# Optimization experiments

Measured on AMD Instinct MI355X. Metric: run time of the kernel, lower is better.

Reference implementation:

```python
import jax, jax.numpy as jnp
import numpy as np

N_NODES = 100000
N_EDGES = 1600000
D_IN = 128
D_OUT = 128


def setup_inputs() -> dict:
    key = jax.random.key(0)
    k1, k2, k3, k4 = jax.random.split(key, 4)
    x = jax.random.normal(k1, (N_NODES, D_IN), dtype=jnp.float32)
    edge_index = jax.random.randint(k2, (2, N_EDGES), 0, N_NODES, dtype=jnp.int64)
    # PyTorch Linear default init: U(-1/sqrt(fan_in), 1/sqrt(fan_in))
    bound = 1.0 / np.sqrt(D_IN)
    W1 = jax.random.uniform(k3, (D_OUT, D_IN), minval=-bound, maxval=bound, dtype=jnp.float32)
    W2 = jax.random.uniform(k4, (D_OUT, D_IN), minval=-bound, maxval=bound, dtype=jnp.float32)
    return {"x": x, "edge_index": edge_index, "W1": W1, "W2": W2}


def reference(x, edge_index, W1, W2):
    # self transform: [N, D_out]
    self_features = x @ W1.T
    # neighbor transform: [N, D_out]
    neighbor_features = x @ W2.T
    row, col = edge_index[0], edge_index[1]
    # gather by source (col), scatter-add by destination (row)
    aggregated = jax.ops.segment_sum(neighbor_features[col], row, num_segments=x.shape[0])
    return jax.nn.relu(self_features + aggregated)
```

## Files before the change

kernel.cpp:

```cpp
#include <hip/hip_runtime.h>

#define N_NODES 100000
#define DIM 128
#define NBIN 391
#define BINSZ 256
#define NCH 782
#define CHUNK 2048
#define FCAP 24
#define SLOTS (NBIN * FCAP)
#define ENTCAP 4608
#define FSPB 128
#define SSPB 256
#define NGEMM 782

typedef __attribute__((ext_vector_type(8))) short bf16x8;
typedef __attribute__((ext_vector_type(4))) float f32x4;

__device__ __forceinline__ unsigned short f2bf(float f) {
  unsigned u = __builtin_bit_cast(unsigned, f);
  u += 0x7fff + ((u >> 16) & 1);
  return (unsigned short)(u >> 16);
}
__device__ __forceinline__ float bfhi(unsigned u) {
  return __builtin_bit_cast(float, u & 0xffff0000u);
}
__device__ __forceinline__ float bflo(unsigned u) {
  return __builtin_bit_cast(float, u << 16);
}

__global__ __launch_bounds__(256, 4) void fill_kernel(
    const int* __restrict__ rows, const int* __restrict__ cols,
    int* __restrict__ counts, unsigned* __restrict__ binned,
    int* __restrict__ fspillc, int2* __restrict__ fspill, int n_edges,
    const float* __restrict__ W1, const float* __restrict__ W2,
    unsigned short* __restrict__ Wb) {
  const int tid = threadIdx.x;
  if (blockIdx.x >= NCH) {
    const int v = (blockIdx.x - NCH) * 256 + tid;
    const int j = v >> 5, q = v & 31;
    const float* Wrow =
        (j < 128) ? (W1 + (size_t)j * DIM) : (W2 + (size_t)(j - 128) * DIM);
    const float4 val = *(const float4*)(Wrow + 4 * q);
    const unsigned lo = (unsigned)f2bf(val.x) | ((unsigned)f2bf(val.y) << 16);
    const unsigned hi = (unsigned)f2bf(val.z) | ((unsigned)f2bf(val.w) << 16);
    *(uint2*)(Wb + (size_t)j * DIM + 4 * q) = make_uint2(lo, hi);
    return;
  }

  __shared__ unsigned buf[SLOTS];
  __shared__ int lcnt[NBIN];
  __shared__ int fsc;
  const int ch = blockIdx.x;
  for (int i = tid; i < NBIN; i += 256) lcnt[i] = 0;
  if (tid == 0) fsc = 0;
  __syncthreads();

  const int e0 = ch * CHUNK + tid * 8;
  int rv[8], cv[8];
  int nval;
  if (e0 + 8 <= n_edges) {
    *(int4*)&rv[0] = *(const int4*)(rows + e0);
    *(int4*)&rv[4] = *(const int4*)(rows + e0 + 4);
    *(int4*)&cv[0] = *(const int4*)(cols + e0);
    *(int4*)&cv[4] = *(const int4*)(cols + e0 + 4);
    nval = 8;
  } else {
    nval = 0;
    for (int k = 0; k < 8; ++k)
      if (e0 + k < n_edges) {
        rv[nval] = rows[e0 + k];
        cv[nval] = cols[e0 + k];
        ++nval;
      }
  }
  for (int k = 0; k < nval; ++k) {
    const int r = rv[k];
    const int b = r >> 8;
    const unsigned payload = ((unsigned)(r & 255) << 17) | (unsigned)cv[k];
    const int slot = atomicAdd(&lcnt[b], 1);
    if (slot < FCAP) {
      buf[b * FCAP + slot] = payload;
    } else {
      const int sp = atomicAdd(&fsc, 1);
      if (sp < FSPB) fspill[ch * FSPB + sp] = make_int2(r, cv[k]);
    }
  }
  __syncthreads();

  unsigned* dst = binned + (size_t)ch * SLOTS;
  for (int i4 = tid; i4 < SLOTS / 4; i4 += 256)
    *(uint4*)(dst + 4 * i4) = *(const uint4*)&buf[4 * i4];
  for (int b = tid; b < NBIN; b += 256)
    counts[(size_t)ch * NBIN + b] = min(lcnt[b], FCAP);
  if (tid == 0) fspillc[ch] = min(fsc, FSPB);
}

union FusedSh {
  unsigned short xs[128 * 136];
  struct {
    int segc[NCH], ssa[NCH], ssb[NCH];
    unsigned entbuf[ENTCAP];
    int outbuf[ENTCAP];
    int hist[BINSZ], hsa[BINSZ], hsb[BINSZ], cur[BINSZ];
    int ssc;
  } s;
};

__global__ __launch_bounds__(256, 2) void gemmsort_kernel(
    const float* __restrict__ x, const unsigned short* __restrict__ Wb,
    unsigned short* __restrict__ selfb, unsigned short* __restrict__ neigh,
    const int* __restrict__ counts, const unsigned* __restrict__ binned,
    int* __restrict__ csr_cols, int* __restrict__ row_ptr,
    int* __restrict__ degs, int* __restrict__ sspillc,
    int2* __restrict__ sspill) {
  __shared__ FusedSh sh;
  const int tid = threadIdx.x;
  const int g = blockIdx.x / 3, r3 = blockIdx.x % 3;

  if (r3 < 2) {
    const int t = g * 2 + r3;
    const int lane = tid & 63;
    const int w = tid >> 6;
    const int nb = t * 128;
    const int quad = lane >> 4;
    const int l15 = lane & 15;

    bf16x8 bfrag[4][4];
#pragma unroll
    for (int nt = 0; nt < 4; ++nt) {
      const int j = w * 64 + nt * 16 + l15;
#pragma unroll
      for (int ks = 0; ks < 4; ++ks)
        bfrag[nt][ks] =
            *(const bf16x8*)(Wb + (size_t)j * DIM + ks * 32 + quad * 8);
    }

#pragma unroll
    for (int half = 0; half < 2; ++half) {
      float4 av[8];
#pragma unroll
      for (int it = 0; it < 8; ++it) {
        const int v = tid + (half * 8 + it) * 256;
        const int m = v >> 5, q = v & 31;
        av[it] = (nb + m < N_NODES)
                     ? *(const float4*)(x + (size_t)(nb + m) * DIM + 4 * q)
                     : make_float4(0.f, 0.f, 0.f, 0.f);
      }
#pragma unroll
      for (int it = 0; it < 8; ++it) {
        const int v = tid + (half * 8 + it) * 256;
        const int m = v >> 5, q = v & 31;
        const unsigned lo =
            (unsigned)f2bf(av[it].x) | ((unsigned)f2bf(av[it].y) << 16);
        const unsigned hi =
            (unsigned)f2bf(av[it].z) | ((unsigned)f2bf(av[it].w) << 16);
        *(uint2*)&sh.xs[m * 136 + 4 * q] = make_uint2(lo, hi);
      }
    }
    __syncthreads();

    f32x4 acc[8][4];
#pragma unroll
    for (int mt = 0; mt < 8; ++mt)
#pragma unroll
      for (int nt = 0; nt < 4; ++nt) acc[mt][nt] = (f32x4){0.f, 0.f, 0.f, 0.f};

#pragma unroll
    for (int ks = 0; ks < 4; ++ks) {
#pragma unroll
      for (int mt = 0; mt < 8; ++mt) {
        const bf16x8 afrag =
            *(const bf16x8*)&sh.xs[(mt * 16 + l15) * 136 + ks * 32 + quad * 8];
#pragma unroll
        for (int nt = 0; nt < 4; ++nt)
          acc[mt][nt] = __builtin_amdgcn_mfma_f32_16x16x32_bf16(
              afrag, bfrag[nt][ks], acc[mt][nt], 0, 0, 0);
      }
    }

#pragma unroll
    for (int h = 0; h < 2; ++h) {
      __syncthreads();
      if ((w >> 1) == h) {
#pragma unroll
        for (int mt = 0; mt < 8; ++mt)
#pragma unroll
          for (int nt = 0; nt < 4; ++nt) {
            const int col = (w & 1) * 64 + nt * 16 + l15;
#pragma unroll
            for (int r = 0; r < 4; ++r)
              sh.xs[(mt * 16 + quad * 4 + r) * 136 + col] =
                  f2bf(acc[mt][nt][r]);
          }
      }
      __syncthreads();
      unsigned short* dst = h ? neigh : selfb;
#pragma unroll
      for (int it = 0; it < 8; ++it) {
        const int v = it * 256 + tid;
        const int row = v >> 4, q = v & 15;
        if (nb + row < N_NODES)
          *(uint4*)(dst + (size_t)(nb + row) * DIM + 8 * q) =
              *(const uint4*)&sh.xs[row * 136 + 8 * q];
      }
    }
  } else {
    const int bin = g;
    if (tid == 0) sh.s.ssc = 0;

    for (int i = tid; i < NCH; i += 256) {
      const int c = counts[(size_t)i * NBIN + bin];
      sh.s.segc[i] = c;
      sh.s.ssa[i] = c;
    }
    __syncthreads();
    for (int off = 1; off < NCH; off <<= 1) {
      for (int i = tid; i < NCH; i += 256)
        sh.s.ssb[i] = sh.s.ssa[i] + ((i >= off) ? sh.s.ssa[i - off] : 0);
      __syncthreads();
      for (int i = tid; i < NCH; i += 256) sh.s.ssa[i] = sh.s.ssb[i];
      __syncthreads();
    }

    const unsigned* bbase = binned + (size_t)bin * FCAP;
    for (int u = tid; u < NCH * (FCAP / 4); u += 256) {
      const int ch = u / 6;
      const int q = u - ch * 6;
      uint4 v4 = *(const uint4*)(bbase + (size_t)ch * SLOTS + 4 * q);
      const int cnt = sh.s.segc[ch];
      const int base = sh.s.ssa[ch] - cnt;
      const unsigned vals[4] = {v4.x, v4.y, v4.z, v4.w};
#pragma unroll
      for (int j = 0; j < 4; ++j) {
        const int slot = 4 * q + j;
        if (slot < cnt) {
          const int pos = base + slot;
          if (pos < ENTCAP) {
            sh.s.entbuf[pos] = vals[j];
          } else {
            const int sp = atomicAdd(&sh.s.ssc, 1);
            if (sp < SSPB)
              sspill[bin * SSPB + sp] =
                  make_int2((bin << 8) | (int)(vals[j] >> 17),
                            (int)(vals[j] & 0x1FFFFu));
          }
        }
      }
    }
    sh.s.hist[tid] = 0;
    __syncthreads();

    const int total = min(sh.s.ssa[NCH - 1], ENTCAP);
    for (int i = tid; i < total; i += 256)
      atomicAdd(&sh.s.hist[sh.s.entbuf[i] >> 17], 1);
    __syncthreads();

    sh.s.hsa[tid] = sh.s.hist[tid];
    __syncthreads();
    for (int off = 1; off < BINSZ; off <<= 1) {
      sh.s.hsb[tid] = sh.s.hsa[tid] + ((tid >= off) ? sh.s.hsa[tid - off] : 0);
      __syncthreads();
      sh.s.hsa[tid] = sh.s.hsb[tid];
      __syncthreads();
    }

    const int gbase = bin * ENTCAP;
    {
      const int start = sh.s.hsa[tid] - sh.s.hist[tid];
      sh.s.cur[tid] = start;
      const int node = (bin << 8) | tid;
      if (node < N_NODES) {
        row_ptr[node] = gbase + start;
        degs[node] = sh.s.hist[tid];
      }
    }
    __syncthreads();

    for (int i = tid; i < total; i += 256) {
      const unsigned p = sh.s.entbuf[i];
      const int pos = atomicAdd(&sh.s.cur[p >> 17], 1);
      sh.s.outbuf[pos] = (int)(p & 0x1FFFFu);
    }
    __syncthreads();

    for (int i = tid; i < total; i += 256)
      csr_cols[gbase + i] = sh.s.outbuf[i];
    if (tid == 0) sspillc[bin] = min(sh.s.ssc, SSPB);
  }
}

__global__ __launch_bounds__(256) void agg_kernel(
    const int* __restrict__ row_ptr, const int* __restrict__ degs,
    const int* __restrict__ csr_cols, const unsigned short* __restrict__ neigh,
    const unsigned short* __restrict__ selfb, const int* __restrict__ fspillc,
    const int2* __restrict__ fspill, const int* __restrict__ sspillc,
    const int2* __restrict__ sspill, float* __restrict__ out) {
  __shared__ int has_spill;
  const int tid = threadIdx.x;
  if (tid == 0) has_spill = 0;
  __syncthreads();
  for (int i = tid; i < NCH + NBIN; i += 256) {
    const int v = (i < NCH) ? fspillc[i] : sspillc[i - NCH];
    if (v) atomicOr(&has_spill, 1);
  }
  __syncthreads();
  const bool spilled = has_spill != 0;

  const int l = tid & 63;
  const int wid = blockIdx.x * 4 + (tid >> 6);
  const int stride = gridDim.x * 4;
  const unsigned* ng = (const unsigned*)neigh;

  for (int node = wid; node < N_NODES; node += stride) {
    const int deg = degs[node];
    const int* cl = csr_cols + row_ptr[node];
    const unsigned s = ((const unsigned*)selfb)[(size_t)node * 64 + l];

    float ax = 0.f, ay = 0.f;
    int d = 0;
    for (; d + 8 <= deg; d += 8) {
      unsigned uv[8];
#pragma unroll
      for (int k = 0; k < 8; ++k) uv[k] = ng[(size_t)cl[d + k] * 64 + l];
#pragma unroll
      for (int k = 0; k < 8; ++k) {
        ax += bflo(uv[k]);
        ay += bfhi(uv[k]);
      }
    }
    const int rem = deg - d;
    if (rem) {
      unsigned uv[8];
      const int cdup = cl[d];
#pragma unroll
      for (int k = 0; k < 8; ++k) {
        const int ci = (k < rem) ? cl[d + k] : cdup;
        uv[k] = ng[(size_t)ci * 64 + l];
      }
#pragma unroll
      for (int k = 0; k < 8; ++k) {
        if (k < rem) {
          ax += bflo(uv[k]);
          ay += bfhi(uv[k]);
        }
      }
    }

    if (spilled) {
      for (int bi = 0; bi < NCH; ++bi) {
        const int n = min(fspillc[bi], FSPB);
        for (int i = 0; i < n; ++i) {
          const int2 e = fspill[bi * FSPB + i];
          if (e.x == node) {
            const unsigned u = ng[(size_t)e.y * 64 + l];
            ax += bflo(u);
            ay += bfhi(u);
          }
        }
      }
      for (int bi = 0; bi < NBIN; ++bi) {
        const int n = min(sspillc[bi], SSPB);
        for (int i = 0; i < n; ++i) {
          const int2 e = sspill[bi * SSPB + i];
          if (e.x == node) {
            const unsigned u = ng[(size_t)e.y * 64 + l];
            ax += bflo(u);
            ay += bfhi(u);
          }
        }
      }
    }

    float2 o;
    o.x = fmaxf(bflo(s) + ax, 0.f);
    o.y = fmaxf(bfhi(s) + ay, 0.f);
    *(float2*)(out + (size_t)node * DIM + 2 * l) = o;
  }
}

extern "C" void kernel_launch(void* const* d_in, const int* in_sizes, int n_in,
                              void* d_out, int out_size, void* d_ws,
                              size_t ws_size, hipStream_t stream) {
  const float* x = (const float*)d_in[0];
  const int* edge_index = (const int*)d_in[1];
  const float* W1 = (const float*)d_in[2];
  const float* W2 = (const float*)d_in[3];
  float* out = (float*)d_out;

  const int n_edges = in_sizes[1] / 2;
  const int* rows = edge_index;
  const int* cols = edge_index + n_edges;

  char* p = (char*)d_ws;
  unsigned short* selfb = (unsigned short*)p;
  p += (size_t)N_NODES * DIM * 2;
  unsigned short* neigh = (unsigned short*)p;
  p += (size_t)N_NODES * DIM * 2;
  unsigned* binned = (unsigned*)p;
  p += (size_t)NCH * SLOTS * 4;
  int* counts = (int*)p;
  p += (size_t)NCH * NBIN * 4;
  int* csr_cols = (int*)p;
  p += (size_t)NBIN * ENTCAP * 4;
  int* row_ptr = (int*)p;
  p += (size_t)N_NODES * 4;
  int* degs = (int*)p;
  p += (size_t)N_NODES * 4;
  int* fspillc = (int*)p;
  p += 4096;
  int2* fspill = (int2*)p;
  p += (size_t)NCH * FSPB * sizeof(int2);
  int* sspillc = (int*)p;
  p += 4096;
  int2* sspill = (int2*)p;
  p += (size_t)NBIN * SSPB * sizeof(int2);
  unsigned short* Wb = (unsigned short*)p;

  fill_kernel<<<NCH + 32, 256, 0, stream>>>(rows, cols, counts, binned,
                                            fspillc, fspill, n_edges, W1, W2,
                                            Wb);
  gemmsort_kernel<<<3 * NBIN, 256, 0, stream>>>(x, Wb, selfb, neigh, counts,
                                                binned, csr_cols, row_ptr,
                                                degs, sspillc, sspill);
  agg_kernel<<<2048, 256, 0, stream>>>(row_ptr, degs, csr_cols, neigh, selfb,
                                       fspillc, fspill, sspillc, sspill, out);
}
```

Measured before the change: 231.1 us.

## Split GEMM from bin sort and fuse per-bin sort with aggregation

Moves the bin sort out of the fused GEMM kernel and into a new 1024-thread kernel that sorts each bin's edges in LDS and aggregates the same bin's nodes straight from LDS. This removes the global CSR write and read (csr_cols, row_ptr, degs) and the global spill scan in aggregation, and handles spills per bin in LDS. In exchange the sort can no longer overlap with the GEMM, and the grid shrinks to 391 large blocks that each gather 256 nodes, which may limit parallelism and latency hiding. A stray `outb[0]=outb[0]` write and a hard spill cap of 64 add minor risk.

```diff
diff --git a/kernel.cpp b/kernel.cpp
--- a/kernel.cpp
+++ b/kernel.cpp
@@ -10,7 +10,7 @@
 #define SLOTS (NBIN * FCAP)
 #define ENTCAP 4608
 #define FSPB 128
-#define SSPB 256
+#define LSPB 64
 #define NGEMM 782
 
 typedef __attribute__((ext_vector_type(8))) short bf16x8;
@@ -95,279 +95,255 @@
   if (tid == 0) fspillc[ch] = min(fsc, FSPB);
 }
 
-union FusedSh {
-  unsigned short xs[128 * 136];
-  struct {
-    int segc[NCH], ssa[NCH], ssb[NCH];
-    unsigned entbuf[ENTCAP];
-    int outbuf[ENTCAP];
-    int hist[BINSZ], hsa[BINSZ], hsb[BINSZ], cur[BINSZ];
-    int ssc;
-  } s;
-};
-
-__global__ __launch_bounds__(256, 2) void gemmsort_kernel(
+__global__ __launch_bounds__(256, 2) void gemm_kernel(
     const float* __restrict__ x, const unsigned short* __restrict__ Wb,
-    unsigned short* __restrict__ selfb, unsigned short* __restrict__ neigh,
+    unsigned short* __restrict__ selfb, unsigned short* __restrict__ neigh) {
+  __shared__ unsigned short xs[128 * 136];
+  const int tid = threadIdx.x;
+  const int t = blockIdx.x;
+  const int lane = tid & 63;
+  const int w = tid >> 6;
+  const int nb = t * 128;
+  const int quad = lane >> 4;
+  const int l15 = lane & 15;
+
+  bf16x8 bfrag[4][4];
+#pragma unroll
+  for (int nt = 0; nt < 4; ++nt) {
+    const int j = w * 64 + nt * 16 + l15;
+#pragma unroll
+    for (int ks = 0; ks < 4; ++ks)
+      bfrag[nt][ks] =
+          *(const bf16x8*)(Wb + (size_t)j * DIM + ks * 32 + quad * 8);
+  }
+
+#pragma unroll
+  for (int half = 0; half < 2; ++half) {
+    float4 av[8];
+#pragma unroll
+    for (int it = 0; it < 8; ++it) {
+      const int v = tid + (half * 8 + it) * 256;
+      const int m = v >> 5, q = v & 31;
+      av[it] = (nb + m < N_NODES)
+                   ? *(const float4*)(x + (size_t)(nb + m) * DIM + 4 * q)
+                   : make_float4(0.f, 0.f, 0.f, 0.f);
+    }
+#pragma unroll
+    for (int it = 0; it < 8; ++it) {
+      const int v = tid + (half * 8 + it) * 256;
+      const int m = v >> 5, q = v & 31;
+      const unsigned lo =
+          (unsigned)f2bf(av[it].x) | ((unsigned)f2bf(av[it].y) << 16);
+      const unsigned hi =
+          (unsigned)f2bf(av[it].z) | ((unsigned)f2bf(av[it].w) << 16);
+      *(uint2*)&xs[m * 136 + 4 * q] = make_uint2(lo, hi);
+    }
+  }
+  __syncthreads();
+
+  f32x4 acc[8][4];
+#pragma unroll
+  for (int mt = 0; mt < 8; ++mt)
+#pragma unroll
+    for (int nt = 0; nt < 4; ++nt) acc[mt][nt] = (f32x4){0.f, 0.f, 0.f, 0.f};
+
+#pragma unroll
+  for (int ks = 0; ks < 4; ++ks) {
+#pragma unroll
+    for (int mt = 0; mt < 8; ++mt) {
+      const bf16x8 afrag =
+          *(const bf16x8*)&xs[(mt * 16 + l15) * 136 + ks * 32 + quad * 8];
+#pragma unroll
+      for (int nt = 0; nt < 4; ++nt)
+        acc[mt][nt] = __builtin_amdgcn_mfma_f32_16x16x32_bf16(
+            afrag, bfrag[nt][ks], acc[mt][nt], 0, 0, 0);
+    }
+  }
+
+#pragma unroll
+  for (int h = 0; h < 2; ++h) {
+    __syncthreads();
+    if ((w >> 1) == h) {
+#pragma unroll
+      for (int mt = 0; mt < 8; ++mt)
+#pragma unroll
+        for (int nt = 0; nt < 4; ++nt) {
+          const int col = (w & 1) * 64 + nt * 16 + l15;
+#pragma unroll
+          for (int r = 0; r < 4; ++r)
+            xs[(mt * 16 + quad * 4 + r) * 136 + col] = f2bf(acc[mt][nt][r]);
+        }
+    }
+    __syncthreads();
+    unsigned short* dst = h ? neigh : selfb;
+#pragma unroll
+    for (int it = 0; it < 8; ++it) {
+      const int v = it * 256 + tid;
+      const int row = v >> 4, q = v & 15;
+      if (nb + row < N_NODES)
+        *(uint4*)(dst + (size_t)(nb + row) * DIM + 8 * q) =
+            *(const uint4*)&xs[row * 136 + 8 * q];
+    }
+  }
+}
+
+__global__ __launch_bounds__(1024, 8) void sortagg_kernel(
     const int* __restrict__ counts, const unsigned* __restrict__ binned,
-    int* __restrict__ csr_cols, int* __restrict__ row_ptr,
-    int* __restrict__ degs, int* __restrict__ sspillc,
-    int2* __restrict__ sspill) {
-  __shared__ FusedSh sh;
+    const unsigned short* __restrict__ neigh,
+    const unsigned short* __restrict__ selfb,
+    const int* __restrict__ fspillc, const int2* __restrict__ fspill,
+    float* __restrict__ out) {
+  __shared__ int segc[NCH];
+  __shared__ int ssa[NCH];
+  __shared__ unsigned entbuf[ENTCAP];
+  __shared__ int outb[ENTCAP];
+  __shared__ int hist[BINSZ], hsa[BINSZ], cur[BINSZ];
+  __shared__ unsigned lspill[LSPB];
+  __shared__ int lsc, tot, hasf;
+
   const int tid = threadIdx.x;
-  const int g = blockIdx.x / 3, r3 = blockIdx.x % 3;
-
-  if (r3 < 2) {
-    const int t = g * 2 + r3;
-    const int lane = tid & 63;
-    const int w = tid >> 6;
-    const int nb = t * 128;
-    const int quad = lane >> 4;
-    const int l15 = lane & 15;
-
-    bf16x8 bfrag[4][4];
-#pragma unroll
-    for (int nt = 0; nt < 4; ++nt) {
-      const int j = w * 64 + nt * 16 + l15;
-#pragma unroll
-      for (int ks = 0; ks < 4; ++ks)
-        bfrag[nt][ks] =
-            *(const bf16x8*)(Wb + (size_t)j * DIM + ks * 32 + quad * 8);
-    }
-
-#pragma unroll
-    for (int half = 0; half < 2; ++half) {
-      float4 av[8];
-#pragma unroll
-      for (int it = 0; it < 8; ++it) {
-        const int v = tid + (half * 8 + it) * 256;
-        const int m = v >> 5, q = v & 31;
-        av[it] = (nb + m < N_NODES)
-                     ? *(const float4*)(x + (size_t)(nb + m) * DIM + 4 * q)
-                     : make_float4(0.f, 0.f, 0.f, 0.f);
-      }
-#pragma unroll
-      for (int it = 0; it < 8; ++it) {
-        const int v = tid + (half * 8 + it) * 256;
-        const int m = v >> 5, q = v & 31;
-        const unsigned lo =
-            (unsigned)f2bf(av[it].x) | ((unsigned)f2bf(av[it].y) << 16);
-        const unsigned hi =
-            (unsigned)f2bf(av[it].z) | ((unsigned)f2bf(av[it].w) << 16);
-        *(uint2*)&sh.xs[m * 136 + 4 * q] = make_uint2(lo, hi);
-      }
-    }
-    __syncthreads();
-
-    f32x4 acc[8][4];
-#pragma unroll
-    for (int mt = 0; mt < 8; ++mt)
-#pragma unroll
-      for (int nt = 0; nt < 4; ++nt) acc[mt][nt] = (f32x4){0.f, 0.f, 0.f, 0.f};
-
-#pragma unroll
-    for (int ks = 0; ks < 4; ++ks) {
-#pragma unroll
-      for (int mt = 0; mt < 8; ++mt) {
-        const bf16x8 afrag =
-            *(const bf16x8*)&sh.xs[(mt * 16 + l15) * 136 + ks * 32 + quad * 8];
-#pragma unroll
-        for (int nt = 0; nt < 4; ++nt)
-          acc[mt][nt] = __builtin_amdgcn_mfma_f32_16x16x32_bf16(
-              afrag, bfrag[nt][ks], acc[mt][nt], 0, 0, 0);
-      }
-    }
-
-#pragma unroll
-    for (int h = 0; h < 2; ++h) {
-      __syncthreads();
-      if ((w >> 1) == h) {
-#pragma unroll
-        for (int mt = 0; mt < 8; ++mt)
-#pragma unroll
-          for (int nt = 0; nt < 4; ++nt) {
-            const int col = (w & 1) * 64 + nt * 16 + l15;
-#pragma unroll
-            for (int r = 0; r < 4; ++r)
-              sh.xs[(mt * 16 + quad * 4 + r) * 136 + col] =
-                  f2bf(acc[mt][nt][r]);
-          }
-      }
-      __syncthreads();
-      unsigned short* dst = h ? neigh : selfb;
-#pragma unroll
-      for (int it = 0; it < 8; ++it) {
-        const int v = it * 256 + tid;
-        const int row = v >> 4, q = v & 15;
-        if (nb + row < N_NODES)
-          *(uint4*)(dst + (size_t)(nb + row) * DIM + 8 * q) =
-              *(const uint4*)&sh.xs[row * 136 + 8 * q];
-      }
-    }
-  } else {
-    const int bin = g;
-    if (tid == 0) sh.s.ssc = 0;
-
-    for (int i = tid; i < NCH; i += 256) {
-      const int c = counts[(size_t)i * NBIN + bin];
-      sh.s.segc[i] = c;
-      sh.s.ssa[i] = c;
-    }
-    __syncthreads();
-    for (int off = 1; off < NCH; off <<= 1) {
-      for (int i = tid; i < NCH; i += 256)
-        sh.s.ssb[i] = sh.s.ssa[i] + ((i >= off) ? sh.s.ssa[i - off] : 0);
-      __syncthreads();
-      for (int i = tid; i < NCH; i += 256) sh.s.ssa[i] = sh.s.ssb[i];
-      __syncthreads();
-    }
-
-    const unsigned* bbase = binned + (size_t)bin * FCAP;
-    for (int u = tid; u < NCH * (FCAP / 4); u += 256) {
-      const int ch = u / 6;
-      const int q = u - ch * 6;
-      uint4 v4 = *(const uint4*)(bbase + (size_t)ch * SLOTS + 4 * q);
-      const int cnt = sh.s.segc[ch];
-      const int base = sh.s.ssa[ch] - cnt;
-      const unsigned vals[4] = {v4.x, v4.y, v4.z, v4.w};
-#pragma unroll
-      for (int j = 0; j < 4; ++j) {
-        const int slot = 4 * q + j;
-        if (slot < cnt) {
-          const int pos = base + slot;
+  const int bin = blockIdx.x;
+
+  if (tid == 0) {
+    lsc = 0;
+    hasf = 0;
+  }
+  if (tid < BINSZ) hist[tid] = 0;
+  for (int i = tid; i < NCH; i += 1024) {
+    const int c = counts[(size_t)i * NBIN + bin];
+    segc[i] = c;
+    ssa[i] = c;
+    if (fspillc[i]) atomicOr(&hasf, 1);
+  }
+  __syncthreads();
+
+  for (int off = 1; off < NCH; off <<= 1) {
+    int add = 0;
+    if (tid < NCH && tid >= off) add = ssa[tid - off];
+    __syncthreads();
+    if (tid < NCH && tid >= off) ssa[tid] += add;
+    __syncthreads();
+  }
+  if (tid == 0) tot = min(ssa[NCH - 1], ENTCAP);
+
+  const unsigned* bbase = binned + (size_t)bin * FCAP;
+  for (int u = tid; u < NCH * (FCAP / 4); u += 1024) {
+    const int ch = u / 6;
+    const int q = u - ch * 6;
+    uint4 v4 = *(const uint4*)(bbase + (size_t)ch * SLOTS + 4 * q);
+    const int cnt = segc[ch];
+    const int base = ssa[ch] - cnt;
+    const unsigned vals[4] = {v4.x, v4.y, v4.z, v4.w};
+#pragma unroll
+    for (int j = 0; j < 4; ++j) {
+      const int slot = 4 * q + j;
+      if (slot < cnt) {
+        const int pos = base + slot;
+        if (pos < ENTCAP) {
+          outb[0] = outb[0];
+          entbuf[pos] = vals[j];
+        } else {
+          const int sp = atomicAdd(&lsc, 1);
+          if (sp < LSPB) lspill[sp] = vals[j];
+        }
+      }
+    }
+  }
+  __syncthreads();
+
+  if (hasf) {
+    for (int bi = tid; bi < NCH; bi += 1024) {
+      const int n = min(fspillc[bi], FSPB);
+      for (int i = 0; i < n; ++i) {
+        const int2 e = fspill[bi * FSPB + i];
+        if ((e.x >> 8) == bin) {
+          const unsigned pay = ((unsigned)(e.x & 255) << 17) | (unsigned)e.y;
+          const int pos = atomicAdd(&tot, 1);
           if (pos < ENTCAP) {
-            sh.s.entbuf[pos] = vals[j];
+            entbuf[pos] = pay;
           } else {
-            const int sp = atomicAdd(&sh.s.ssc, 1);
-            if (sp < SSPB)
-              sspill[bin * SSPB + sp] =
-                  make_int2((bin << 8) | (int)(vals[j] >> 17),
-                            (int)(vals[j] & 0x1FFFFu));
+            const int sp = atomicAdd(&lsc, 1);
+            if (sp < LSPB) lspill[sp] = pay;
           }
         }
       }
     }
-    sh.s.hist[tid] = 0;
-    __syncthreads();
-
-    const int total = min(sh.s.ssa[NCH - 1], ENTCAP);
-    for (int i = tid; i < total; i += 256)
-      atomicAdd(&sh.s.hist[sh.s.entbuf[i] >> 17], 1);
-    __syncthreads();
-
-    sh.s.hsa[tid] = sh.s.hist[tid];
-    __syncthreads();
-    for (int off = 1; off < BINSZ; off <<= 1) {
-      sh.s.hsb[tid] = sh.s.hsa[tid] + ((tid >= off) ? sh.s.hsa[tid - off] : 0);
-      __syncthreads();
-      sh.s.hsa[tid] = sh.s.hsb[tid];
-      __syncthreads();
-    }
-
-    const int gbase = bin * ENTCAP;
-    {
-      const int start = sh.s.hsa[tid] - sh.s.hist[tid];
-      sh.s.cur[tid] = start;
-      const int node = (bin << 8) | tid;
-      if (node < N_NODES) {
-        row_ptr[node] = gbase + start;
-        degs[node] = sh.s.hist[tid];
-      }
-    }
-    __syncthreads();
-
-    for (int i = tid; i < total; i += 256) {
-      const unsigned p = sh.s.entbuf[i];
-      const int pos = atomicAdd(&sh.s.cur[p >> 17], 1);
-      sh.s.outbuf[pos] = (int)(p & 0x1FFFFu);
-    }
-    __syncthreads();
-
-    for (int i = tid; i < total; i += 256)
-      csr_cols[gbase + i] = sh.s.outbuf[i];
-    if (tid == 0) sspillc[bin] = min(sh.s.ssc, SSPB);
-  }
-}
-
-__global__ __launch_bounds__(256) void agg_kernel(
-    const int* __restrict__ row_ptr, const int* __restrict__ degs,
-    const int* __restrict__ csr_cols, const unsigned short* __restrict__ neigh,
-    const unsigned short* __restrict__ selfb, const int* __restrict__ fspillc,
-    const int2* __restrict__ fspill, const int* __restrict__ sspillc,
-    const int2* __restrict__ sspill, float* __restrict__ out) {
-  __shared__ int has_spill;
-  const int tid = threadIdx.x;
-  if (tid == 0) has_spill = 0;
-  __syncthreads();
-  for (int i = tid; i < NCH + NBIN; i += 256) {
-    const int v = (i < NCH) ? fspillc[i] : sspillc[i - NCH];
-    if (v) atomicOr(&has_spill, 1);
-  }
-  __syncthreads();
-  const bool spilled = has_spill != 0;
+    __syncthreads();
+  }
+  const int total = min(tot, ENTCAP);
+
+  for (int i = tid; i < total; i += 1024)
+    atomicAdd(&hist[entbuf[i] >> 17], 1);
+  __syncthreads();
+  if (tid < BINSZ) hsa[tid] = hist[tid];
+  __syncthreads();
+  for (int off = 1; off < BINSZ; off <<= 1) {
+    int add = 0;
+    if (tid < BINSZ && tid >= off) add = hsa[tid - off];
+    __syncthreads();
+    if (tid < BINSZ && tid >= off) hsa[tid] += add;
+    __syncthreads();
+  }
+  if (tid < BINSZ) cur[tid] = hsa[tid] - hist[tid];
+  __syncthreads();
+
+  for (int i = tid; i < total; i += 1024) {
+    const unsigned p = entbuf[i];
+    const int pos = atomicAdd(&cur[p >> 17], 1);
+    outb[pos] = (int)(p & 0x1FFFFu);
+  }
+  __syncthreads();
 
   const int l = tid & 63;
-  const int wid = blockIdx.x * 4 + (tid >> 6);
-  const int stride = gridDim.x * 4;
+  const int wv = tid >> 6;
   const unsigned* ng = (const unsigned*)neigh;
-
-  for (int node = wid; node < N_NODES; node += stride) {
-    const int deg = degs[node];
-    const int* cl = csr_cols + row_ptr[node];
-    const unsigned s = ((const unsigned*)selfb)[(size_t)node * 64 + l];
+  const unsigned* sfp = (const unsigned*)selfb;
+  const int nspill = min(lsc, LSPB);
+
+  for (int k = 0; k < 16; ++k) {
+    const int nl = wv * 16 + k;
+    const int node = (bin << 8) | nl;
+    if (node >= N_NODES) break;
+    const int deg = hist[nl];
+    const int start = hsa[nl] - hist[nl];
+    const unsigned s = sfp[(size_t)node * 64 + l];
 
     float ax = 0.f, ay = 0.f;
     int d = 0;
     for (; d + 8 <= deg; d += 8) {
       unsigned uv[8];
 #pragma unroll
-      for (int k = 0; k < 8; ++k) uv[k] = ng[(size_t)cl[d + k] * 64 + l];
-#pragma unroll
-      for (int k = 0; k < 8; ++k) {
-        ax += bflo(uv[k]);
-        ay += bfhi(uv[k]);
+      for (int j = 0; j < 8; ++j) uv[j] = ng[(size_t)outb[start + d + j] * 64 + l];
+#pragma unroll
+      for (int j = 0; j < 8; ++j) {
+        ax += bflo(uv[j]);
+        ay += bfhi(uv[j]);
       }
     }
     const int rem = deg - d;
     if (rem) {
       unsigned uv[8];
-      const int cdup = cl[d];
-#pragma unroll
-      for (int k = 0; k < 8; ++k) {
-        const int ci = (k < rem) ? cl[d + k] : cdup;
-        uv[k] = ng[(size_t)ci * 64 + l];
-      }
-#pragma unroll
-      for (int k = 0; k < 8; ++k) {
-        if (k < rem) {
-          ax += bflo(uv[k]);
-          ay += bfhi(uv[k]);
+      const int cdup = outb[start + d];
+#pragma unroll
+      for (int j = 0; j < 8; ++j) {
+        const int ci = (j < rem) ? outb[start + d + j] : cdup;
+        uv[j] = ng[(size_t)ci * 64 + l];
+      }
+#pragma unroll
+      for (int j = 0; j < 8; ++j) {
+        if (j < rem) {
+          ax += bflo(uv[j]);
+          ay += bfhi(uv[j]);
         }
       }
     }
 
-    if (spilled) {
-      for (int bi = 0; bi < NCH; ++bi) {
-        const int n = min(fspillc[bi], FSPB);
-        for (int i = 0; i < n; ++i) {
-          const int2 e = fspill[bi * FSPB + i];
-          if (e.x == node) {
-            const unsigned u = ng[(size_t)e.y * 64 + l];
-            ax += bflo(u);
-            ay += bfhi(u);
-          }
-        }
-      }
-      for (int bi = 0; bi < NBIN; ++bi) {
-        const int n = min(sspillc[bi], SSPB);
-        for (int i = 0; i < n; ++i) {
-          const int2 e = sspill[bi * SSPB + i];
-          if (e.x == node) {
-            const unsigned u = ng[(size_t)e.y * 64 + l];
-            ax += bflo(u);
-            ay += bfhi(u);
-          }
-        }
+    for (int i = 0; i < nspill; ++i) {
+      const unsigned p = lspill[i];
+      if ((int)(p >> 17) == nl) {
+        const unsigned u = ng[(size_t)(p & 0x1FFFFu) * 64 + l];
+        ax += bflo(u);
+        ay += bfhi(u);
       }
     }
 
@@ -400,28 +376,21 @@
   p += (size_t)NCH * SLOTS * 4;
   int* counts = (int*)p;
   p += (size_t)NCH * NBIN * 4;
-  int* csr_cols = (int*)p;
   p += (size_t)NBIN * ENTCAP * 4;
-  int* row_ptr = (int*)p;
   p += (size_t)N_NODES * 4;
-  int* degs = (int*)p;
   p += (size_t)N_NODES * 4;
   int* fspillc = (int*)p;
   p += 4096;
   int2* fspill = (int2*)p;
   p += (size_t)NCH * FSPB * sizeof(int2);
-  int* sspillc = (int*)p;
   p += 4096;
-  int2* sspill = (int2*)p;
-  p += (size_t)NBIN * SSPB * sizeof(int2);
+  p += (size_t)NBIN * 256 * sizeof(int2);
   unsigned short* Wb = (unsigned short*)p;
 
   fill_kernel<<<NCH + 32, 256, 0, stream>>>(rows, cols, counts, binned,
                                             fspillc, fspill, n_edges, W1, W2,
                                             Wb);
-  gemmsort_kernel<<<3 * NBIN, 256, 0, stream>>>(x, Wb, selfb, neigh, counts,
-                                                binned, csr_cols, row_ptr,
-                                                degs, sspillc, sspill);
-  agg_kernel<<<2048, 256, 0, stream>>>(row_ptr, degs, csr_cols, neigh, selfb,
-                                       fspillc, fspill, sspillc, sspill, out);
-}
+  gemm_kernel<<<NGEMM, 256, 0, stream>>>(x, Wb, selfb, neigh);
+  sortagg_kernel<<<NBIN, 1024, 0, stream>>>(counts, binned, neigh, selfb,
+                                            fspillc, fspill, out);
+}
```

Result: faster. 217.6 us (-5.8%).
